# Kernel optimization log

Measured on AMD Instinct MI355X. Metric: run time of the kernel, lower is better.

Reference implementation:

```python
import jax, jax.numpy as jnp
import numpy as np

B, N, T, F_IN, H, E = 64, 325, 24, 64, 64, 2600
NEG_SLOPE = 0.2


def setup_inputs() -> dict:
    key = jax.random.key(0)
    k1, k2, k3, k4, k5 = jax.random.split(key, 5)
    x = jax.random.normal(k1, (B, N, T, F_IN), dtype=jnp.float32)
    edge_index = jax.random.randint(k2, (2, E), 0, N, dtype=jnp.int32)
    scale = 1.0 / np.sqrt(F_IN)
    W = jax.random.normal(k3, (H, F_IN), dtype=jnp.float32) * scale
    att_src = jax.random.normal(k4, (H,), dtype=jnp.float32) * scale
    att_dst = jax.random.normal(k5, (H,), dtype=jnp.float32) * scale
    bias = jnp.zeros((H,), dtype=jnp.float32)
    return {"x": x, "edge_index": edge_index, "W": W,
            "att_src": att_src, "att_dst": att_dst, "bias": bias}


def reference(x, edge_index, W, att_src, att_dst, bias):
    b, n, t, nf = x.shape
    # Fold the B*T graph replicas into one leading axis: [G, N, F]
    xg = x.transpose(0, 2, 1, 3).reshape(b * t, n, nf)
    h = jnp.einsum('gnf,hf->gnh', xg, W)  # linear transform [G, N, H]
    a_s = h @ att_src  # [G, N] per-node source attention logit
    a_d = h @ att_dst  # [G, N] per-node dest attention logit
    src, dst = edge_index[0], edge_index[1]
    # Per-edge raw score (gather), LeakyReLU as in GATConv: [G, E]
    e = jax.nn.leaky_relu(a_s[:, src] + a_d[:, dst], negative_slope=NEG_SLOPE)

    def per_graph(e_g, h_g):
        # segment softmax over edges grouped by destination node
        m = jax.ops.segment_max(e_g, dst, num_segments=n)
        ex = jnp.exp(e_g - m[dst])
        den = jax.ops.segment_sum(ex, dst, num_segments=n)
        alpha = ex / den[dst]  # [E]
        msg = alpha[:, None] * h_g[src]  # [E, H]
        return jax.ops.segment_sum(msg, dst, num_segments=n)  # [N, H]

    out = jax.vmap(per_graph)(e, h) + bias  # [G, N, H]
    out = jax.nn.gelu(out, approximate=False)
    # Faithful to source: view(B,T,N,H) then raw reshape(B,N,T,H) (row-major reinterpret)
    return out.reshape(b, n, t, -1)
```

## Files before the change

kernel.cpp:

```cpp
#include <hip/hip_runtime.h>
#include <hip/hip_bf16.h>

#define B_  64
#define N_  325
#define T_  24
#define F_  64
#define H_  64
#define E_  2600
#define G_  (B_ * T_)
#define BLK 512
#define GRID3 512
#define HS  72

using half2_t = __attribute__((ext_vector_type(2))) _Float16;
using half8_t = __attribute__((ext_vector_type(8))) _Float16;
using f32x4   = __attribute__((ext_vector_type(4))) float;

__global__ __launch_bounds__(512) void k_off_prep(
    const int* __restrict__ ei, const float* __restrict__ W,
    const float* __restrict__ att_src, const float* __restrict__ att_dst,
    int* __restrict__ csr_off, unsigned short* __restrict__ perm,
    float* __restrict__ w_sd) {
  __shared__ int cnt[N_];
  const int tid = threadIdx.x;
  for (int i = tid; i < N_; i += BLK) cnt[i] = 0;
  __syncthreads();
  for (int e = tid; e < E_; e += BLK) atomicAdd(&cnt[ei[E_ + e]], 1);
  __syncthreads();
  if (tid <= N_) {
    int off = 0;
    for (int m = 0; m < N_; ++m) off += (m < tid) ? cnt[m] : 0;
    csr_off[tid] = off;
  }
  if (tid < N_) {
    const int c = cnt[tid];
    int r = 0;
    for (int m = 0; m < N_; ++m) {
      const int cm = cnt[m];
      r += (cm > c || (cm == c && m < tid)) ? 1 : 0;
    }
    perm[r] = (unsigned short)tid;
  }
  if (tid < 128) {
    const int k = tid & 63;
    const float* av = (tid < 64) ? att_src : att_dst;
    float s = 0.f;
    for (int h = 0; h < H_; ++h) s += W[h * F_ + k] * av[h];
    w_sd[tid] = s;
  }
}

__global__ __launch_bounds__(64) void k_scatter(const int* __restrict__ ei,
                                                const int* __restrict__ csr_off,
                                                unsigned short* __restrict__ csr_src,
                                                unsigned short* __restrict__ edst) {
  __shared__ int dsts[E_];
  const int tid = threadIdx.x;
  for (int i = tid; i < E_; i += 64) dsts[i] = ei[E_ + i];
  __syncthreads();
  const int e = blockIdx.x * 64 + tid;
  if (e >= E_) return;
  const int myd = dsts[e];
  int rank = 0;
#pragma unroll 4
  for (int k = 0; k < e; ++k) rank += (dsts[k] == myd) ? 1 : 0;
  const int pos = csr_off[myd] + rank;
  csr_src[pos] = (unsigned short)ei[e];
  edst[pos]    = (unsigned short)myd;
}

__device__ __forceinline__ float f16lo(unsigned u) {
  half2_t h = __builtin_bit_cast(half2_t, u); return (float)h[0];
}
__device__ __forceinline__ float f16hi(unsigned u) {
  half2_t h = __builtin_bit_cast(half2_t, u); return (float)h[1];
}
__device__ __forceinline__ unsigned short f16b(float f) {
  _Float16 h = (_Float16)f; return __builtin_bit_cast(unsigned short, h);
}
__device__ __forceinline__ half2_t pkrtz(float a, float b) {
  return __builtin_bit_cast(half2_t, __builtin_amdgcn_cvt_pkrtz(a, b));
}
__device__ __forceinline__ half2_t bch2(unsigned u) {
  return __builtin_bit_cast(half2_t, u);
}
__device__ __forceinline__ half8_t pk8(float4 a, float4 b) {
  half2_t p0 = pkrtz(a.x, a.y);
  half2_t p1 = pkrtz(a.z, a.w);
  half2_t p2 = pkrtz(b.x, b.y);
  half2_t p3 = pkrtz(b.z, b.w);
  half8_t r;
  r[0] = p0[0]; r[1] = p0[1]; r[2] = p1[0]; r[3] = p1[1];
  r[4] = p2[0]; r[5] = p2[1]; r[6] = p3[0]; r[7] = p3[1];
  return r;
}

__device__ __forceinline__ float gelu_f(float v) {
  float t = v * (1.5957691216f + 0.0713550903f * (v * v));
  t = fminf(t, 80.0f);
  float e = __expf(t);
  return v * e * __builtin_amdgcn_rcpf(e + 1.0f);
}

__global__ __launch_bounds__(512, 4) void k_gat13(
    const float* __restrict__ x, const int* __restrict__ csr_off_g,
    const unsigned short* __restrict__ csr_src_g,
    const unsigned short* __restrict__ perm_g,
    const unsigned short* __restrict__ edst_g, const float* __restrict__ W,
    const float* __restrict__ w_sd, const float* __restrict__ bias,
    float* __restrict__ out) {
  __shared__ __align__(16) _Float16 h_s[N_][HS];
  __shared__ uint2    edge_s[E_];
  __shared__ unsigned short edst_s[E_];
  __shared__ unsigned asad_s[N_];
  __shared__ unsigned short coff_s[N_ + 1];
  __shared__ unsigned short perm_s[N_];

  const int tid  = threadIdx.x;
  const int lane = tid & 63;
  const int wv   = tid >> 6;
  const int l15  = lane & 15;
  const int l4   = lane >> 4;

  for (int i = tid; i < E_; i += BLK) {
    edge_s[i] = make_uint2(0u, (unsigned)csr_src_g[i]);
    edst_s[i] = edst_g[i];
  }
  for (int i = tid; i <= N_; i += BLK) coff_s[i] = csr_off_g[i];
  for (int i = tid; i < N_; i += BLK) perm_s[i] = perm_g[i];

  half8_t bf[2][4];
#pragma unroll
  for (int ct = 0; ct < 4; ++ct)
#pragma unroll
    for (int k0 = 0; k0 < 2; ++k0) {
      const float* p = W + (size_t)(ct * 16 + l15) * F_ + k0 * 32 + l4 * 8;
      bf[k0][ct] = pk8(*(const float4*)p, *(const float4*)(p + 4));
    }

  half8_t bw[2];
  {
    const float* wp = w_sd + (l15 & 1) * 64;
#pragma unroll
    for (int k0 = 0; k0 < 2; ++k0) {
      half8_t z = {0, 0, 0, 0, 0, 0, 0, 0};
      const float* p = wp + k0 * 32 + l4 * 8;
      bw[k0] = (l15 < 2) ? pk8(*(const float4*)p, *(const float4*)(p + 4)) : z;
    }
  }

  const int l8 = tid & 7;
  const int gq = tid >> 3;
  const float4 biasA = *(const float4*)(bias + 8 * l8);
  const float4 biasB = *(const float4*)(bias + 8 * l8 + 4);

  for (int gi = 0; gi < 3; ++gi) {
    const int g  = blockIdx.x + (gi << 9);
    const int bb = g / T_;
    const int tt = g % T_;
    if (gi) __syncthreads();

    const float* xg = x + ((size_t)bb * N_ * T_ + tt) * F_;
#pragma unroll
    for (int ti = 0; ti < 3; ++ti) {
      const int t = wv + ti * 8;
      int tc = t > 20 ? 20 : t;
      int rr = tc * 16 + l15; if (rr > N_ - 1) rr = N_ - 1;
      const float* xr = xg + (size_t)rr * (T_ * F_) + l4 * 8;
      const float4 u0 = *(const float4*)xr;
      const float4 u1 = *(const float4*)(xr + 4);
      const float4 u2 = *(const float4*)(xr + 32);
      const float4 u3 = *(const float4*)(xr + 36);
      if (t < 21) {
        const int r0 = t * 16;
        const half8_t a0 = pk8(u0, u1);
        const half8_t a1 = pk8(u2, u3);
        const bool full = (r0 + 16 <= N_);
#pragma unroll
        for (int ct = 0; ct < 4; ++ct) {
          f32x4 acc = {0.f, 0.f, 0.f, 0.f};
          acc = __builtin_amdgcn_mfma_f32_16x16x32_f16(a0, bf[0][ct], acc, 0, 0, 0);
          acc = __builtin_amdgcn_mfma_f32_16x16x32_f16(a1, bf[1][ct], acc, 0, 0, 0);
          const int col = ct * 16 + l15;
#pragma unroll
          for (int j = 0; j < 4; ++j) {
            const int row = r0 + l4 * 4 + j;
            if (full || row < N_) h_s[row][col] = (_Float16)acc[j];
          }
        }
        f32x4 acc2 = {0.f, 0.f, 0.f, 0.f};
        acc2 = __builtin_amdgcn_mfma_f32_16x16x32_f16(a0, bw[0], acc2, 0, 0, 0);
        acc2 = __builtin_amdgcn_mfma_f32_16x16x32_f16(a1, bw[1], acc2, 0, 0, 0);
        if (l15 < 2) {
#pragma unroll
          for (int j = 0; j < 4; ++j) {
            const int row = r0 + l4 * 4 + j;
            if (full || row < N_)
              ((unsigned short*)asad_s)[row * 2 + l15] = f16b(acc2[j]);
          }
        }
      }
    }
    __syncthreads();

    {
      unsigned spv[6]; unsigned short dpv[6];
#pragma unroll
      for (int k = 0; k < 6; ++k) {
        const int p = tid + k * BLK;
        spv[k] = (p < E_) ? edge_s[p].y : 0u;
        dpv[k] = (p < E_) ? edst_s[p] : (unsigned short)0;
      }
      float ev[6];
#pragma unroll
      for (int k = 0; k < 6; ++k)
        ev[k] = f16lo(asad_s[spv[k]]) + f16hi(asad_s[dpv[k]]);
#pragma unroll
      for (int k = 0; k < 6; ++k) {
        const int p = tid + k * BLK;
        if (p < E_) {
          float e = fmaxf(ev[k], 0.2f * ev[k]);
          const float ex =
              __builtin_amdgcn_exp2f(__builtin_fmaf(e, 1.44269504f, -7.21347520f));
          const unsigned ax = (unsigned)f16b(ex);
          edge_s[p].x = ax | (ax << 16);
        }
      }
    }
    __syncthreads();

#pragma unroll
    for (int r = 0; r < 6; ++r) {
      const int idx = r * 64 + ((r & 1) ? (63 - gq) : gq);
      if (idx < N_) {
        const int n   = perm_s[idx];
        const int beg = coff_s[n], end = coff_s[n + 1];
        half2_t a01 = {(_Float16)0.f, (_Float16)0.f};
        half2_t a23 = {(_Float16)0.f, (_Float16)0.f};
        half2_t a45 = {(_Float16)0.f, (_Float16)0.f};
        half2_t a67 = {(_Float16)0.f, (_Float16)0.f};
        float den = 0.f;
        int p = beg;
        for (; p + 4 <= end; p += 4) {
          const uint2 e0 = edge_s[p];
          const uint2 e1 = edge_s[p + 1];
          const uint2 e2 = edge_s[p + 2];
          const uint2 e3 = edge_s[p + 3];
          const uint4 h0 = *(const uint4*)&h_s[e0.y][8 * l8];
          const uint4 h1 = *(const uint4*)&h_s[e1.y][8 * l8];
          const uint4 h2 = *(const uint4*)&h_s[e2.y][8 * l8];
          const uint4 h3 = *(const uint4*)&h_s[e3.y][8 * l8];
          den += f16lo(e0.x) + f16lo(e1.x) + f16lo(e2.x) + f16lo(e3.x);
          const half2_t al0 = bch2(e0.x), al1 = bch2(e1.x);
          const half2_t al2 = bch2(e2.x), al3 = bch2(e3.x);
          a01 = al0 * bch2(h0.x) + a01; a23 = al0 * bch2(h0.y) + a23;
          a45 = al0 * bch2(h0.z) + a45; a67 = al0 * bch2(h0.w) + a67;
          a01 = al1 * bch2(h1.x) + a01; a23 = al1 * bch2(h1.y) + a23;
          a45 = al1 * bch2(h1.z) + a45; a67 = al1 * bch2(h1.w) + a67;
          a01 = al2 * bch2(h2.x) + a01; a23 = al2 * bch2(h2.y) + a23;
          a45 = al2 * bch2(h2.z) + a45; a67 = al2 * bch2(h2.w) + a67;
          a01 = al3 * bch2(h3.x) + a01; a23 = al3 * bch2(h3.y) + a23;
          a45 = al3 * bch2(h3.z) + a45; a67 = al3 * bch2(h3.w) + a67;
        }
        for (; p < end; ++p) {
          const uint2 eu = edge_s[p];
          den += f16lo(eu.x);
          const half2_t al = bch2(eu.x);
          const uint4 hv = *(const uint4*)&h_s[eu.y][8 * l8];
          a01 = al * bch2(hv.x) + a01; a23 = al * bch2(hv.y) + a23;
          a45 = al * bch2(hv.z) + a45; a67 = al * bch2(hv.w) + a67;
        }
        const float inv = (end > beg) ? __builtin_amdgcn_rcpf(den) : 0.0f;
        const float v0 = gelu_f((float)a01[0] * inv + biasA.x);
        const float v1 = gelu_f((float)a01[1] * inv + biasA.y);
        const float v2 = gelu_f((float)a23[0] * inv + biasA.z);
        const float v3 = gelu_f((float)a23[1] * inv + biasA.w);
        const float v4 = gelu_f((float)a45[0] * inv + biasB.x);
        const float v5 = gelu_f((float)a45[1] * inv + biasB.y);
        const float v6 = gelu_f((float)a67[0] * inv + biasB.z);
        const float v7 = gelu_f((float)a67[1] * inv + biasB.w);
        float* op = &out[((size_t)g * N_ + n) * H_ + 8 * l8];
        *(float4*)op       = make_float4(v0, v1, v2, v3);
        *(float4*)(op + 4) = make_float4(v4, v5, v6, v7);
      }
    }
  }
}

extern "C" void kernel_launch(void* const* d_in, const int* in_sizes, int n_in,
                              void* d_out, int out_size, void* d_ws, size_t ws_size,
                              hipStream_t stream) {
  (void)in_sizes; (void)n_in; (void)out_size; (void)ws_size;
  const float* x       = (const float*)d_in[0];
  const int*   ei      = (const int*)d_in[1];
  const float* W       = (const float*)d_in[2];
  const float* att_src = (const float*)d_in[3];
  const float* att_dst = (const float*)d_in[4];
  const float* bias    = (const float*)d_in[5];
  float* out = (float*)d_out;

  char* ws = (char*)d_ws;
  int*            csr_off = (int*)(ws + 0);
  unsigned short* csr_src = (unsigned short*)(ws + 4096);
  unsigned short* perm    = (unsigned short*)(ws + 16384);
  unsigned short* edst    = (unsigned short*)(ws + 20480);
  float*          w_sd    = (float*)(ws + 28672);

  k_off_prep<<<1, BLK, 0, stream>>>(ei, W, att_src, att_dst, csr_off, perm, w_sd);
  k_scatter<<<(E_ + 63) / 64, 64, 0, stream>>>(ei, csr_off, csr_src, edst);
  k_gat13<<<GRID3, BLK, 0, stream>>>(x, csr_off, csr_src, perm, edst, W, w_sd,
                                     bias, out);
}
```

Before: 107.7 us.

## Replace per-node gather aggregation with MFMA over dense per-tile attention blocks

The neighbour aggregation step now stores h transposed and, for each 16-destination tile, builds a dense 16x32 attention sub-matrix in LDS via shared atomics over source chunks. It then multiplies that sub-matrix with h on MFMA, getting the denominator from a ones column. This replaces the scalar half2 FMA gather loop and removes the degree-sorted permutation. The cost is 11 source chunks per tile, each with an LDS zero/atomic/read round trip, so much of the MFMA work runs over zeros. Edges per tile are assumed to be at most 256, since only 4 edges per lane are loaded.

```diff
diff --git a/kernel.cpp b/kernel.cpp
--- a/kernel.cpp
+++ b/kernel.cpp
@@ -10,7 +10,7 @@
 #define G_  (B_ * T_)
 #define BLK 512
 #define GRID3 512
-#define HS  72
+#define HT  328
 
 using half2_t = __attribute__((ext_vector_type(2))) _Float16;
 using half8_t = __attribute__((ext_vector_type(8))) _Float16;
@@ -19,8 +19,7 @@
 __global__ __launch_bounds__(512) void k_off_prep(
     const int* __restrict__ ei, const float* __restrict__ W,
     const float* __restrict__ att_src, const float* __restrict__ att_dst,
-    int* __restrict__ csr_off, unsigned short* __restrict__ perm,
-    float* __restrict__ w_sd) {
+    int* __restrict__ csr_off, float* __restrict__ w_sd) {
   __shared__ int cnt[N_];
   const int tid = threadIdx.x;
   for (int i = tid; i < N_; i += BLK) cnt[i] = 0;
@@ -31,15 +30,6 @@
     int off = 0;
     for (int m = 0; m < N_; ++m) off += (m < tid) ? cnt[m] : 0;
     csr_off[tid] = off;
-  }
-  if (tid < N_) {
-    const int c = cnt[tid];
-    int r = 0;
-    for (int m = 0; m < N_; ++m) {
-      const int cm = cnt[m];
-      r += (cm > c || (cm == c && m < tid)) ? 1 : 0;
-    }
-    perm[r] = (unsigned short)tid;
   }
   if (tid < 128) {
     const int k = tid & 63;
@@ -78,11 +68,11 @@
 __device__ __forceinline__ unsigned short f16b(float f) {
   _Float16 h = (_Float16)f; return __builtin_bit_cast(unsigned short, h);
 }
+__device__ __forceinline__ float f16u(unsigned short u) {
+  return (float)__builtin_bit_cast(_Float16, u);
+}
 __device__ __forceinline__ half2_t pkrtz(float a, float b) {
   return __builtin_bit_cast(half2_t, __builtin_amdgcn_cvt_pkrtz(a, b));
-}
-__device__ __forceinline__ half2_t bch2(unsigned u) {
-  return __builtin_bit_cast(half2_t, u);
 }
 __device__ __forceinline__ half8_t pk8(float4 a, float4 b) {
   half2_t p0 = pkrtz(a.x, a.y);
@@ -102,19 +92,19 @@
   return v * e * __builtin_amdgcn_rcpf(e + 1.0f);
 }
 
-__global__ __launch_bounds__(512, 4) void k_gat13(
+__global__ __launch_bounds__(512, 4) void k_gat14(
     const float* __restrict__ x, const int* __restrict__ csr_off_g,
     const unsigned short* __restrict__ csr_src_g,
-    const unsigned short* __restrict__ perm_g,
     const unsigned short* __restrict__ edst_g, const float* __restrict__ W,
     const float* __restrict__ w_sd, const float* __restrict__ bias,
     float* __restrict__ out) {
-  __shared__ __align__(16) _Float16 h_s[N_][HS];
-  __shared__ uint2    edge_s[E_];
+  __shared__ __align__(16) _Float16 hT[65 * HT];
+  __shared__ __align__(16) float Pbuf[8 * 16 * 32];
+  __shared__ unsigned epk[E_];
   __shared__ unsigned short edst_s[E_];
   __shared__ unsigned asad_s[N_];
   __shared__ unsigned short coff_s[N_ + 1];
-  __shared__ unsigned short perm_s[N_];
+  __shared__ float bias_s[H_];
 
   const int tid  = threadIdx.x;
   const int lane = tid & 63;
@@ -122,12 +112,17 @@
   const int l15  = lane & 15;
   const int l4   = lane >> 4;
 
+  {
+    const f32x4 z4 = {0.f, 0.f, 0.f, 0.f};
+    f32x4* hz = (f32x4*)hT;
+    for (int i = tid; i < 2665; i += BLK) hz[i] = z4;
+  }
   for (int i = tid; i < E_; i += BLK) {
-    edge_s[i] = make_uint2(0u, (unsigned)csr_src_g[i]);
+    epk[i] = (unsigned)csr_src_g[i];
     edst_s[i] = edst_g[i];
   }
   for (int i = tid; i <= N_; i += BLK) coff_s[i] = csr_off_g[i];
-  for (int i = tid; i < N_; i += BLK) perm_s[i] = perm_g[i];
+  if (tid < H_) bias_s[tid] = bias[tid];
 
   half8_t bf[2][4];
 #pragma unroll
@@ -137,7 +132,6 @@
       const float* p = W + (size_t)(ct * 16 + l15) * F_ + k0 * 32 + l4 * 8;
       bf[k0][ct] = pk8(*(const float4*)p, *(const float4*)(p + 4));
     }
-
   half8_t bw[2];
   {
     const float* wp = w_sd + (l15 & 1) * 64;
@@ -148,11 +142,10 @@
       bw[k0] = (l15 < 2) ? pk8(*(const float4*)p, *(const float4*)(p + 4)) : z;
     }
   }
-
-  const int l8 = tid & 7;
-  const int gq = tid >> 3;
-  const float4 biasA = *(const float4*)(bias + 8 * l8);
-  const float4 biasB = *(const float4*)(bias + 8 * l8 + 4);
+  half8_t ones;
+#pragma unroll
+  for (int i = 0; i < 8; ++i) ones[i] = (_Float16)1.0f;
+  __syncthreads();
 
   for (int gi = 0; gi < 3; ++gi) {
     const int g  = blockIdx.x + (gi << 9);
@@ -181,11 +174,11 @@
           f32x4 acc = {0.f, 0.f, 0.f, 0.f};
           acc = __builtin_amdgcn_mfma_f32_16x16x32_f16(a0, bf[0][ct], acc, 0, 0, 0);
           acc = __builtin_amdgcn_mfma_f32_16x16x32_f16(a1, bf[1][ct], acc, 0, 0, 0);
-          const int col = ct * 16 + l15;
+          const int ch = ct * 16 + l15;
 #pragma unroll
           for (int j = 0; j < 4; ++j) {
             const int row = r0 + l4 * 4 + j;
-            if (full || row < N_) h_s[row][col] = (_Float16)acc[j];
+            if (full || row < N_) hT[ch * HT + row] = (_Float16)acc[j];
           }
         }
         f32x4 acc2 = {0.f, 0.f, 0.f, 0.f};
@@ -208,13 +201,13 @@
 #pragma unroll
       for (int k = 0; k < 6; ++k) {
         const int p = tid + k * BLK;
-        spv[k] = (p < E_) ? edge_s[p].y : 0u;
+        spv[k] = (p < E_) ? epk[p] : 0u;
         dpv[k] = (p < E_) ? edst_s[p] : (unsigned short)0;
       }
       float ev[6];
 #pragma unroll
       for (int k = 0; k < 6; ++k)
-        ev[k] = f16lo(asad_s[spv[k]]) + f16hi(asad_s[dpv[k]]);
+        ev[k] = f16lo(asad_s[spv[k] & 0xffffu]) + f16hi(asad_s[dpv[k]]);
 #pragma unroll
       for (int k = 0; k < 6; ++k) {
         const int p = tid + k * BLK;
@@ -222,66 +215,67 @@
           float e = fmaxf(ev[k], 0.2f * ev[k]);
           const float ex =
               __builtin_amdgcn_exp2f(__builtin_fmaf(e, 1.44269504f, -7.21347520f));
-          const unsigned ax = (unsigned)f16b(ex);
-          edge_s[p].x = ax | (ax << 16);
+          epk[p] = (spv[k] & 0xffffu) | ((unsigned)f16b(ex) << 16);
         }
       }
     }
     __syncthreads();
 
-#pragma unroll
-    for (int r = 0; r < 6; ++r) {
-      const int idx = r * 64 + ((r & 1) ? (63 - gq) : gq);
-      if (idx < N_) {
-        const int n   = perm_s[idx];
-        const int beg = coff_s[n], end = coff_s[n + 1];
-        half2_t a01 = {(_Float16)0.f, (_Float16)0.f};
-        half2_t a23 = {(_Float16)0.f, (_Float16)0.f};
-        half2_t a45 = {(_Float16)0.f, (_Float16)0.f};
-        half2_t a67 = {(_Float16)0.f, (_Float16)0.f};
-        float den = 0.f;
-        int p = beg;
-        for (; p + 4 <= end; p += 4) {
-          const uint2 e0 = edge_s[p];
-          const uint2 e1 = edge_s[p + 1];
-          const uint2 e2 = edge_s[p + 2];
-          const uint2 e3 = edge_s[p + 3];
-          const uint4 h0 = *(const uint4*)&h_s[e0.y][8 * l8];
-          const uint4 h1 = *(const uint4*)&h_s[e1.y][8 * l8];
-          const uint4 h2 = *(const uint4*)&h_s[e2.y][8 * l8];
-          const uint4 h3 = *(const uint4*)&h_s[e3.y][8 * l8];
-          den += f16lo(e0.x) + f16lo(e1.x) + f16lo(e2.x) + f16lo(e3.x);
-          const half2_t al0 = bch2(e0.x), al1 = bch2(e1.x);
-          const half2_t al2 = bch2(e2.x), al3 = bch2(e3.x);
-          a01 = al0 * bch2(h0.x) + a01; a23 = al0 * bch2(h0.y) + a23;
-          a45 = al0 * bch2(h0.z) + a45; a67 = al0 * bch2(h0.w) + a67;
-          a01 = al1 * bch2(h1.x) + a01; a23 = al1 * bch2(h1.y) + a23;
-          a45 = al1 * bch2(h1.z) + a45; a67 = al1 * bch2(h1.w) + a67;
-          a01 = al2 * bch2(h2.x) + a01; a23 = al2 * bch2(h2.y) + a23;
-          a45 = al2 * bch2(h2.z) + a45; a67 = al2 * bch2(h2.w) + a67;
-          a01 = al3 * bch2(h3.x) + a01; a23 = al3 * bch2(h3.y) + a23;
-          a45 = al3 * bch2(h3.z) + a45; a67 = al3 * bch2(h3.w) + a67;
-        }
-        for (; p < end; ++p) {
-          const uint2 eu = edge_s[p];
-          den += f16lo(eu.x);
-          const half2_t al = bch2(eu.x);
-          const uint4 hv = *(const uint4*)&h_s[eu.y][8 * l8];
-          a01 = al * bch2(hv.x) + a01; a23 = al * bch2(hv.y) + a23;
-          a45 = al * bch2(hv.z) + a45; a67 = al * bch2(hv.w) + a67;
-        }
-        const float inv = (end > beg) ? __builtin_amdgcn_rcpf(den) : 0.0f;
-        const float v0 = gelu_f((float)a01[0] * inv + biasA.x);
-        const float v1 = gelu_f((float)a01[1] * inv + biasA.y);
-        const float v2 = gelu_f((float)a23[0] * inv + biasA.z);
-        const float v3 = gelu_f((float)a23[1] * inv + biasA.w);
-        const float v4 = gelu_f((float)a45[0] * inv + biasB.x);
-        const float v5 = gelu_f((float)a45[1] * inv + biasB.y);
-        const float v6 = gelu_f((float)a67[0] * inv + biasB.z);
-        const float v7 = gelu_f((float)a67[1] * inv + biasB.w);
-        float* op = &out[((size_t)g * N_ + n) * H_ + 8 * l8];
-        *(float4*)op       = make_float4(v0, v1, v2, v3);
-        *(float4*)(op + 4) = make_float4(v4, v5, v6, v7);
+    float* Pw = Pbuf + wv * 512;
+    for (int t = wv; t < 21; t += 8) {
+      const int dlo = t * 16;
+      const int dhi = (dlo + 16 < N_) ? dlo + 16 : N_;
+      const int ebeg = coff_s[dlo], eend = coff_s[dhi];
+      unsigned ea[4]; int ed[4];
+#pragma unroll
+      for (int k = 0; k < 4; ++k) {
+        const int p = ebeg + lane + k * 64;
+        const bool v = p < eend;
+        ea[k] = v ? epk[p] : 0u;
+        ed[k] = v ? (edst_s[p] & 15) : 0;
+      }
+      f32x4 ac0 = {0.f, 0.f, 0.f, 0.f}, ac1 = {0.f, 0.f, 0.f, 0.f};
+      f32x4 ac2 = {0.f, 0.f, 0.f, 0.f}, ac3 = {0.f, 0.f, 0.f, 0.f};
+      f32x4 acd = {0.f, 0.f, 0.f, 0.f};
+      for (int kc = 0; kc < 11; ++kc) {
+        const f32x4 z4 = {0.f, 0.f, 0.f, 0.f};
+        *(f32x4*)(Pw + lane * 8) = z4;
+        *(f32x4*)(Pw + lane * 8 + 4) = z4;
+        asm volatile("" ::: "memory");
+        const int s0 = kc * 32;
+#pragma unroll
+        for (int k = 0; k < 4; ++k) {
+          const int sl = (int)(ea[k] & 0xffffu) - s0;
+          if ((unsigned)sl < 32u)
+            atomicAdd(Pw + ed[k] * 32 + sl, f16u((unsigned short)(ea[k] >> 16)));
+        }
+        asm volatile("" ::: "memory");
+        const float4 pa = *(const float4*)(Pw + l15 * 32 + l4 * 8);
+        const float4 pb = *(const float4*)(Pw + l15 * 32 + l4 * 8 + 4);
+        const half8_t af = pk8(pa, pb);
+        const int sb = s0 + l4 * 8;
+        const uint4 b0 = *(const uint4*)&hT[(0 * 16 + l15) * HT + sb];
+        const uint4 b1 = *(const uint4*)&hT[(1 * 16 + l15) * HT + sb];
+        const uint4 b2 = *(const uint4*)&hT[(2 * 16 + l15) * HT + sb];
+        const uint4 b3 = *(const uint4*)&hT[(3 * 16 + l15) * HT + sb];
+        ac0 = __builtin_amdgcn_mfma_f32_16x16x32_f16(af, __builtin_bit_cast(half8_t, b0), ac0, 0, 0, 0);
+        ac1 = __builtin_amdgcn_mfma_f32_16x16x32_f16(af, __builtin_bit_cast(half8_t, b1), ac1, 0, 0, 0);
+        ac2 = __builtin_amdgcn_mfma_f32_16x16x32_f16(af, __builtin_bit_cast(half8_t, b2), ac2, 0, 0, 0);
+        ac3 = __builtin_amdgcn_mfma_f32_16x16x32_f16(af, __builtin_bit_cast(half8_t, b3), ac3, 0, 0, 0);
+        acd = __builtin_amdgcn_mfma_f32_16x16x32_f16(af, ones, acd, 0, 0, 0);
+      }
+#pragma unroll
+      for (int j = 0; j < 4; ++j) {
+        const int row = dlo + l4 * 4 + j;
+        if (row < N_) {
+          const float den = acd[j];
+          const float dinv = (den > 0.f) ? __builtin_amdgcn_rcpf(den) : 0.f;
+          float* orow = out + ((size_t)g * N_ + row) * H_;
+          orow[l15]      = gelu_f(ac0[j] * dinv + bias_s[l15]);
+          orow[16 + l15] = gelu_f(ac1[j] * dinv + bias_s[16 + l15]);
+          orow[32 + l15] = gelu_f(ac2[j] * dinv + bias_s[32 + l15]);
+          orow[48 + l15] = gelu_f(ac3[j] * dinv + bias_s[48 + l15]);
+        }
       }
     }
   }
@@ -302,12 +296,10 @@
   char* ws = (char*)d_ws;
   int*            csr_off = (int*)(ws + 0);
   unsigned short* csr_src = (unsigned short*)(ws + 4096);
-  unsigned short* perm    = (unsigned short*)(ws + 16384);
-  unsigned short* edst    = (unsigned short*)(ws + 20480);
-  float*          w_sd    = (float*)(ws + 28672);
-
-  k_off_prep<<<1, BLK, 0, stream>>>(ei, W, att_src, att_dst, csr_off, perm, w_sd);
+  unsigned short* edst    = (unsigned short*)(ws + 12288);
+  float*          w_sd    = (float*)(ws + 20480);
+
+  k_off_prep<<<1, BLK, 0, stream>>>(ei, W, att_src, att_dst, csr_off, w_sd);
   k_scatter<<<(E_ + 63) / 64, 64, 0, stream>>>(ei, csr_off, csr_src, edst);
-  k_gat13<<<GRID3, BLK, 0, stream>>>(x, csr_off, csr_src, perm, edst, W, w_sd,
-                                     bias, out);
-}
+  k_gat14<<<GRID3, BLK, 0, stream>>>(x, csr_off, csr_src, edst, W, w_sd, bias, out);
+}
```

Result: slower. 216.6 us (+101.1%).
